# Kernel tuning notes

Hardware: AMD Instinct MI355X
Metric: run time of the kernel (lower is better)

The kernel has to match this reference:

```python
import jax, jax.numpy as jnp
import numpy as np

B, N, C = 4, 4096, 1024
H, M = 16, 64          # num_heads, num_landmarks
DH = C // H
SCALE = H ** (-0.5)    # faithful to source: num_heads**-0.5
LN_EPS = 1e-5


def setup_inputs() -> dict:
    key = jax.random.key(0)
    ks = jax.random.split(key, 8)
    s = 0.02
    return {
        "x": jax.random.normal(ks[0], (B, N, C), jnp.float32),
        "ln_w": jnp.ones((C,), jnp.float32),
        "ln_b": jnp.zeros((C,), jnp.float32),
        "qkv_w": jax.random.normal(ks[1], (3 * C, C), jnp.float32) * s,
        "qkv_b": jax.random.normal(ks[2], (3 * C,), jnp.float32) * s,
        "gamma_w": jax.random.normal(ks[3], (C, C), jnp.float32) * s,
        "gamma_b": jax.random.normal(ks[4], (C,), jnp.float32) * s,
        "proj_w": jax.random.normal(ks[5], (C, C), jnp.float32) * s,
        "proj_b": jax.random.normal(ks[6], (C,), jnp.float32) * s,
    }


def _iterative_inv(K, n_iter=6):
    # Newton-Schulz pseudo-inverse on [..., M, M]
    Id = jnp.eye(K.shape[-1], dtype=K.dtype)
    KA = jnp.abs(K)
    V0 = KA.sum(axis=-2, keepdims=True).max(axis=-1, keepdims=True)
    VI = KA.sum(axis=-1, keepdims=True).max(axis=-2, keepdims=True)
    V = jnp.swapaxes(K, -2, -1) / (V0 * VI)
    for _ in range(n_iter):
        KV = K @ V
        V = 0.25 * V @ (13.0 * Id - KV @ (15.0 * Id - KV @ (7.0 * Id - KV)))
    return V


def reference(x, ln_w, ln_b, qkv_w, qkv_b, gamma_w, gamma_b, proj_w, proj_b):
    # LayerNorm
    mu = x.mean(axis=-1, keepdims=True)
    var = x.var(axis=-1, keepdims=True)
    xn = (x - mu) * jax.lax.rsqrt(var + LN_EPS) * ln_w + ln_b
    # qkv: (B,N,3C) -> (3,B,H,N,DH)
    qkv = (xn @ qkv_w.T + qkv_b).reshape(B, N, 3, H, DH).transpose(2, 0, 3, 1, 4)
    q, k, v = qkv[0], qkv[1], qkv[2]
    # landmarks: mean-pool segments of length N//M, then scale
    q_lm = q.reshape(B, H, M, N // M, DH).mean(axis=-2) * SCALE  # (B,H,M,DH)
    k_lm = k.reshape(B, H, M, N // M, DH).mean(axis=-2) * SCALE
    attn1 = jax.nn.softmax(jnp.einsum('bhnd,bhmd->bhnm', q, k_lm), axis=-1)    # (B,H,N,M)
    attn2 = jax.nn.softmax(jnp.einsum('bhmd,bhld->bhml', q_lm, k_lm), axis=-1)  # (B,H,M,M)
    attn3 = jax.nn.softmax(jnp.einsum('bhmd,bhnd->bhmn', q_lm, k), axis=-1)    # (B,H,M,N)
    attn2_inv = _iterative_inv(attn2)
    out = attn1 @ (attn2_inv @ (attn3 @ v))            # (B,H,N,DH)
    out = out.transpose(0, 2, 1, 3).reshape(B, N, C)
    out = out @ gamma_w.T + gamma_b                    # LipNorm=True branch
    out = out @ proj_w.T + proj_b                      # proj (dropout p=0 is identity)
    return out
```

## Files before the change

### kernel.cpp

```cpp
#include <hip/hip_runtime.h>
#include <stdint.h>

typedef unsigned short u16;
typedef short bf16x8 __attribute__((ext_vector_type(8)));
typedef float f32x4 __attribute__((ext_vector_type(4)));

#define MFMA16(a, b, c) __builtin_amdgcn_mfma_f32_16x16x32_bf16((a), (b), (c), 0, 0, 0)

static __device__ __forceinline__ float bfu2f(u16 u) {
  union { unsigned int i; float f; } z; z.i = ((unsigned int)u) << 16; return z.f;
}
static __device__ __forceinline__ u16 f2bfu(float f) {
  union { float f; unsigned int i; } z; z.f = f;
  unsigned int i = z.i;
  return (u16)((i + 0x7fffu + ((i >> 16) & 1u)) >> 16);
}

__device__ __forceinline__ void gload_lds16(const void* g, void* l) {
  __builtin_amdgcn_global_load_lds((const __attribute__((address_space(1))) void*)g,
                                   (__attribute__((address_space(3))) void*)l, 16, 0, 0);
}

__global__ __launch_bounds__(256) void ln_kernel(
    const float* __restrict__ x, const float* __restrict__ w,
    const float* __restrict__ b, u16* __restrict__ xn) {
  int row = blockIdx.x;
  int t = threadIdx.x;
  const float4* xr = (const float4*)(x + (size_t)row * 1024);
  float4 v = xr[t];
  float s = v.x + v.y + v.z + v.w;
  float ss = v.x * v.x + v.y * v.y + v.z * v.z + v.w * v.w;
#pragma unroll
  for (int m = 1; m < 64; m <<= 1) { s += __shfl_xor(s, m); ss += __shfl_xor(ss, m); }
  __shared__ float sb[4], ssb[4];
  int lane = t & 63, wvi = t >> 6;
  if (lane == 0) { sb[wvi] = s; ssb[wvi] = ss; }
  __syncthreads();
  s = sb[0] + sb[1] + sb[2] + sb[3];
  ss = ssb[0] + ssb[1] + ssb[2] + ssb[3];
  float mu = s * (1.0f / 1024.0f);
  float var = ss * (1.0f / 1024.0f) - mu * mu;
  float rstd = rsqrtf(var + 1e-5f);
  float4 wv4 = ((const float4*)w)[t];
  float4 bv4 = ((const float4*)b)[t];
  ushort4 o;
  o.x = f2bfu((v.x - mu) * rstd * wv4.x + bv4.x);
  o.y = f2bfu((v.y - mu) * rstd * wv4.y + bv4.y);
  o.z = f2bfu((v.z - mu) * rstd * wv4.z + bv4.z);
  o.w = f2bfu((v.w - mu) * rstd * wv4.w + bv4.w);
  ((ushort4*)xn)[(size_t)row * 256 + t] = o;
}

__global__ void cvt3_kernel(const float* __restrict__ a, u16* __restrict__ oa, int na,
                            const float* __restrict__ b, u16* __restrict__ ob, int nb,
                            const float* __restrict__ c, u16* __restrict__ oc, int nc) {
  int total = (na + nb + nc) >> 2;
  for (int i = blockIdx.x * blockDim.x + threadIdx.x; i < total; i += gridDim.x * blockDim.x) {
    int j = i << 2;
    const float* s; u16* d; int off;
    if (j < na) { s = a; d = oa; off = j; }
    else if (j < na + nb) { s = b; d = ob; off = j - na; }
    else { s = c; d = oc; off = j - na - nb; }
    float4 v = *(const float4*)(s + off);
    ushort4 o;
    o.x = f2bfu(v.x); o.y = f2bfu(v.y); o.z = f2bfu(v.z); o.w = f2bfu(v.w);
    *(ushort4*)(d + off) = o;
  }
}

template <int MODE>
__global__ __launch_bounds__(512, 2) void gemm_bt(
    const u16* __restrict__ A, const u16* __restrict__ Bw,
    const float* __restrict__ bias,
    float* __restrict__ Cf, u16* __restrict__ Cb,
    u16* __restrict__ Qo, u16* __restrict__ Ko, u16* __restrict__ Vo,
    int M, int N, int K) {
  __shared__ __attribute__((aligned(16))) u16 As[2][16384];
  __shared__ __attribute__((aligned(16))) u16 Bs[2][16384];
  int tid = threadIdx.x;
  int lane = tid & 63;
  int w = tid >> 6;
  int wr = w >> 2, wc = w & 3;
  int r16 = lane & 15, hi = lane >> 4;
  int l8 = lane >> 3, li = lane & 7;

  int nwg = gridDim.x * gridDim.y;
  int flat = blockIdx.y * gridDim.x + blockIdx.x;
  int q8 = nwg >> 3;
  int swz = (flat & 7) * q8 + (flat >> 3);
  int bx = swz % gridDim.x, by = swz / gridDim.x;

  const char* Abase = (const char*)(A + (size_t)by * 256 * K);
  const char* Bbase = (const char*)(Bw + (size_t)bx * 256 * K);
  size_t rowbytes = (size_t)K * 2;
  int colsw = (li ^ l8) << 4;
  int nkt = K >> 6;

  f32x4 z4 = {0.f, 0.f, 0.f, 0.f};
  f32x4 acc[8][4];
#pragma unroll
  for (int m = 0; m < 8; ++m)
#pragma unroll
    for (int n = 0; n < 4; ++n) acc[m][n] = z4;

#define SG_A(buf, t, r0)                                                      \
  gload_lds16(Abase + (size_t)((r0) + w * 8 + l8) * rowbytes + ((t) << 7) +   \
                  colsw,                                                      \
              (char*)As[buf] + ((r0) + w * 8) * 128)
#define SG_B(buf, t, r0)                                                      \
  gload_lds16(Bbase + (size_t)((r0) + w * 8 + l8) * rowbytes + ((t) << 7) +   \
                  colsw,                                                      \
              (char*)Bs[buf] + ((r0) + w * 8) * 128)

  SG_A(0, 0, 0); SG_A(0, 0, 64); SG_A(0, 0, 128); SG_A(0, 0, 192);
  SG_B(0, 0, 0); SG_B(0, 0, 64); SG_B(0, 0, 128); SG_B(0, 0, 192);
  SG_A(1, 1, 0); SG_A(1, 1, 128); SG_B(1, 1, 0); SG_B(1, 1, 64);
  SG_A(1, 1, 64); SG_A(1, 1, 192);
  asm volatile("s_waitcnt vmcnt(6)" ::: "memory");
  __builtin_amdgcn_s_barrier();
  __builtin_amdgcn_sched_barrier(0);

  int buf = 0;
  bf16x8 af[4][2], bfr[4][2];

#define LDA(mh)                                                               \
  _Pragma("unroll") for (int m = 0; m < 4; ++m) {                             \
    int row = wr * 128 + (mh) * 64 + m * 16 + r16;                            \
    int sw = (row & 7) << 4;                                                  \
    _Pragma("unroll") for (int kk = 0; kk < 2; ++kk)                          \
        af[m][kk] = *(const bf16x8*)(ab + row * 128 +                         \
                                     (((kk << 6) | (hi << 4)) ^ sw));         \
  }
#define LDB(nh)                                                               \
  _Pragma("unroll") for (int n = 0; n < 2; ++n) {                             \
    int row = wc * 64 + (nh) * 32 + n * 16 + r16;                             \
    int sw = (row & 7) << 4;                                                  \
    _Pragma("unroll") for (int kk = 0; kk < 2; ++kk)                          \
        bfr[(nh) * 2 + n][kk] = *(const bf16x8*)(ab2 + row * 128 +            \
                                     (((kk << 6) | (hi << 4)) ^ sw));         \
  }
#define MM(mh, nh)                                                            \
  __builtin_amdgcn_s_setprio(1);                                              \
  _Pragma("unroll") for (int kk = 0; kk < 2; ++kk)                            \
      _Pragma("unroll") for (int m = 0; m < 4; ++m)                           \
          _Pragma("unroll") for (int n = 0; n < 2; ++n)                       \
              acc[(mh) * 4 + m][(nh) * 2 + n] =                               \
      MFMA16(af[m][kk], bfr[(nh) * 2 + n][kk], acc[(mh) * 4 + m][(nh) * 2 + n]); \
  __builtin_amdgcn_s_setprio(0)

#define BAR1                                                                  \
  __builtin_amdgcn_s_barrier();                                               \
  __builtin_amdgcn_sched_barrier(0)
#define BAR2                                                                  \
  __builtin_amdgcn_sched_barrier(0);                                          \
  __builtin_amdgcn_s_barrier();                                               \
  __builtin_amdgcn_sched_barrier(0)

  for (int t = 0; t < nkt; ++t) {
    const char* ab = (const char*)As[buf];
    const char* ab2 = (const char*)Bs[buf];
    bool s1 = (t + 1 < nkt), s2 = (t + 2 < nkt);
    LDA(0);
    LDB(0);
    if (s1) { SG_B(buf ^ 1, t + 1, 128); SG_B(buf ^ 1, t + 1, 192); }
    BAR1;
    MM(0, 0);
    BAR2;
    LDB(1);
    if (s2) { SG_A(buf, t + 2, 0); SG_A(buf, t + 2, 128); }
    BAR1;
    MM(0, 1);
    BAR2;
    LDA(1);
    if (s2) { SG_B(buf, t + 2, 0); SG_B(buf, t + 2, 64); }
    BAR1;
    MM(1, 0);
    BAR2;
    if (s2) { SG_A(buf, t + 2, 64); SG_A(buf, t + 2, 192); }
    BAR1;
    MM(1, 1);
    __builtin_amdgcn_sched_barrier(0);
    if (s2) {
      asm volatile("s_waitcnt vmcnt(6)" ::: "memory");
    } else {
      asm volatile("s_waitcnt vmcnt(0)" ::: "memory");
    }
    __builtin_amdgcn_s_barrier();
    __builtin_amdgcn_sched_barrier(0);
    buf ^= 1;
  }
#undef SG_A
#undef SG_B
#undef LDA
#undef LDB
#undef MM
#undef BAR1
#undef BAR2

#pragma unroll
  for (int m = 0; m < 8; ++m)
#pragma unroll
    for (int n = 0; n < 4; ++n) {
      int row0 = by * 256 + wr * 128 + m * 16 + hi * 4;
      int col = bx * 256 + wc * 64 + n * 16 + r16;
      if (MODE == 2) {
        int jt = col >> 10;
        int h = (col >> 6) & 15, dh = col & 63;
        int bb = row0 >> 12, nt0 = row0 & 4095;
        float bcol = bias[col];
        if (jt == 2) {
          ushort4 o;
          o.x = f2bfu(acc[m][n][0] + bcol);
          o.y = f2bfu(acc[m][n][1] + bcol);
          o.z = f2bfu(acc[m][n][2] + bcol);
          o.w = f2bfu(acc[m][n][3] + bcol);
          *(ushort4*)&Vo[(((size_t)bb * 16 + h) * 64 + dh) * 4096 + nt0] = o;
        } else {
          u16* dst = (jt == 0) ? Qo : Ko;
#pragma unroll
          for (int r = 0; r < 4; ++r)
            dst[(((size_t)bb * 16 + h) * 4096 + nt0 + r) * 64 + dh] =
                f2bfu(acc[m][n][r] + bcol);
        }
      } else {
        float bcol = 0.f;
        if constexpr (MODE != 3) bcol = bias[col];
#pragma unroll
        for (int r = 0; r < 4; ++r) {
          int row = row0 + r;
          float val = acc[m][n][r] + bcol;
          if (MODE == 1) Cf[(size_t)row * N + col] = val;
          else           Cb[(size_t)row * N + col] = f2bfu(val);
        }
      }
    }
}

__global__ __launch_bounds__(64) void landmark_kernel(
    const u16* __restrict__ Q, const u16* __restrict__ K,
    float* __restrict__ qlmf, u16* __restrict__ qlmb,
    float* __restrict__ klmf, u16* __restrict__ klmb) {
  int bm = blockIdx.x;
  int bh = bm >> 6, m = bm & 63;
  int l = threadIdx.x;
  const u16* src = blockIdx.y ? K : Q;
  const u16* base = src + (((size_t)bh * 4096) + m * 64) * 64;
  int r0 = l >> 3;
  int c0 = (l & 7) * 8;
  float s[8] = {};
#pragma unroll
  for (int p = 0; p < 8; ++p) {
    bf16x8 v = *(const bf16x8*)(base + (size_t)(r0 + p * 8) * 64 + c0);
#pragma unroll
    for (int j = 0; j < 8; ++j) s[j] += bfu2f((u16)v[j]);
  }
#pragma unroll
  for (int j = 0; j < 8; ++j) {
    s[j] += __shfl_xor(s[j], 8);
    s[j] += __shfl_xor(s[j], 16);
    s[j] += __shfl_xor(s[j], 32);
  }
  if (l < 8) {
    size_t o = (size_t)bh * 4096 + m * 64 + l * 8;
    float* fo = blockIdx.y ? klmf : qlmf;
    u16* bo = blockIdx.y ? klmb : qlmb;
#pragma unroll
    for (int j = 0; j < 8; ++j) {
      float val = s[j] * (0.25f / 64.0f);
      fo[o + j] = val;
      bo[o + j] = f2bfu(val);
    }
  }
}

__global__ __launch_bounds__(256) void attn3_pv_kernel(
    const u16* __restrict__ qlmb, const u16* __restrict__ Kmat,
    const u16* __restrict__ Vt, float* __restrict__ Upart,
    float* __restrict__ rspart) {
  __shared__ __attribute__((aligned(16))) u16 Elds[4][8192];
  int chunk = blockIdx.x, bh = blockIdx.y;
  int tid = threadIdx.x, lane = tid & 63, w = tid >> 6;
  int r16 = lane & 15, hi = lane >> 4;
  int keybase = chunk * 512 + w * 128;
  const u16* kb = Kmat + ((size_t)bh * 4096 + keybase) * 64;
  const u16* vtb = Vt + (size_t)bh * 262144;
  const u16* qb = qlmb + (size_t)bh * 4096;
  u16* eb = &Elds[w][0];
  f32x4 z4 = {0.f, 0.f, 0.f, 0.f};

  bf16x8 afr[4][2];
#pragma unroll
  for (int m = 0; m < 4; ++m)
#pragma unroll
    for (int kk = 0; kk < 2; ++kk)
      afr[m][kk] = *(const bf16x8*)(qb + (m * 16 + r16) * 64 + kk * 32 + hi * 8);

  float rs[4][4] = {};
  for (int cf = 0; cf < 8; ++cf) {
    f32x4 S[4] = {z4, z4, z4, z4};
#pragma unroll
    for (int kk = 0; kk < 2; ++kk) {
      bf16x8 bfr = *(const bf16x8*)(kb + (size_t)(cf * 16 + r16) * 64 + kk * 32 + hi * 8);
#pragma unroll
      for (int m = 0; m < 4; ++m) S[m] = MFMA16(afr[m][kk], bfr, S[m]);
    }
#pragma unroll
    for (int m = 0; m < 4; ++m)
#pragma unroll
      for (int r = 0; r < 4; ++r) {
        float e = __expf(S[m][r]);
        rs[m][r] += e;
        int row = m * 16 + hi * 4 + r;
        int key = cf * 16 + r16;
        *(u16*)((char*)eb + row * 256 + ((key * 2) ^ ((row & 7) << 4))) = f2bfu(e);
      }
  }
#pragma unroll
  for (int m = 0; m < 4; ++m)
#pragma unroll
    for (int r = 0; r < 4; ++r) {
      float v = rs[m][r];
      v += __shfl_xor(v, 1); v += __shfl_xor(v, 2);
      v += __shfl_xor(v, 4); v += __shfl_xor(v, 8);
      rs[m][r] = v;
    }
  if (r16 == 0) {
    float* rp = rspart + (((size_t)bh * 8 + chunk) * 4 + w) * 64;
#pragma unroll
    for (int m = 0; m < 4; ++m)
#pragma unroll
      for (int r = 0; r < 4; ++r) rp[m * 16 + hi * 4 + r] = rs[m][r];
  }
  __syncthreads();

  f32x4 U[4][4];
#pragma unroll
  for (int m = 0; m < 4; ++m)
#pragma unroll
    for (int df = 0; df < 4; ++df) U[m][df] = z4;
  for (int ks = 0; ks < 4; ++ks) {
    bf16x8 ea[4];
#pragma unroll
    for (int m = 0; m < 4; ++m) {
      int row = m * 16 + r16;
      ea[m] = *(const bf16x8*)((char*)eb + row * 256 + (((ks * 32 + hi * 8) * 2) ^ ((row & 7) << 4)));
    }
#pragma unroll
    for (int df = 0; df < 4; ++df) {
      bf16x8 vb8 = *(const bf16x8*)(vtb + (size_t)(df * 16 + r16) * 4096 +
                                    keybase + ks * 32 + hi * 8);
#pragma unroll
      for (int m = 0; m < 4; ++m) U[m][df] = MFMA16(ea[m], vb8, U[m][df]);
    }
  }
  float* up = Upart + (((size_t)bh * 8 + chunk) * 4 + w) * 4096;
#pragma unroll
  for (int m = 0; m < 4; ++m)
#pragma unroll
    for (int df = 0; df < 4; ++df)
#pragma unroll
      for (int r = 0; r < 4; ++r)
        up[(m * 16 + hi * 4 + r) * 64 + df * 16 + r16] = U[m][df][r];
}

__global__ __launch_bounds__(256) void reduce_t_kernel(
    const float* __restrict__ Upart, const float* __restrict__ rspart,
    float* __restrict__ Tmf) {
  int bh = blockIdx.y;
  int tid = threadIdx.x;
  __shared__ float rsum[64];
  if (tid < 64) {
    float s = 0.f;
    const float* rp = rspart + (size_t)bh * 2048 + tid;
#pragma unroll 8
    for (int p = 0; p < 32; ++p) s += rp[p * 64];
    rsum[tid] = s;
  }
  __syncthreads();
  int idx4 = blockIdx.x * 256 + tid;
  const float4* up = (const float4*)(Upart + (size_t)bh * 131072) + idx4;
  float4 s = {0.f, 0.f, 0.f, 0.f};
#pragma unroll 8
  for (int p = 0; p < 32; ++p) {
    float4 v = up[p * 1024];
    s.x += v.x; s.y += v.y; s.z += v.z; s.w += v.w;
  }
  float inv = 1.0f / rsum[idx4 >> 4];
  s.x *= inv; s.y *= inv; s.z *= inv; s.w *= inv;
  ((float4*)(Tmf + (size_t)bh * 4096))[idx4] = s;
}

__global__ __launch_bounds__(256) void transpose_g_kernel(
    const float* __restrict__ G, u16* __restrict__ GT) {
  __shared__ float t[64][65];
  int tr = blockIdx.y * 64, tc = blockIdx.x * 64;
  int l = threadIdx.x & 63, y = threadIdx.x >> 6;
  for (int r = y; r < 64; r += 4)
    t[r][l] = G[(size_t)(tr + r) * 1024 + tc + l];
  __syncthreads();
  for (int rr = y; rr < 64; rr += 4)
    GT[(size_t)(tc + rr) * 1024 + tr + l] = f2bfu(t[l][rr]);
}

__global__ __launch_bounds__(256) void bias2_kernel(
    const float* __restrict__ P, const float* __restrict__ gb,
    const float* __restrict__ pb, float* __restrict__ b2) {
  int i = blockIdx.x * 256 + threadIdx.x;
  const float4* pr = (const float4*)(P + (size_t)i * 1024);
  const float4* g4 = (const float4*)gb;
  float s = 0.f;
  for (int k = 0; k < 256; ++k) {
    float4 a = pr[k], b = g4[k];
    s += a.x * b.x + a.y * b.y + a.z * b.z + a.w * b.w;
  }
  b2[i] = s + pb[i];
}

__device__ __forceinline__ void mm64(const float (*AT)[68], const float (*Bm)[68],
                                     float (*C)[68], float (*CT)[68],
                                     float alpha, int tid) {
  int tr = (tid >> 4) << 2;
  int tc = (tid & 15) << 2;
  float acc[4][4] = {};
#pragma unroll 4
  for (int k = 0; k < 64; ++k) {
    float4 av = *(const float4*)&AT[k][tr];
    float4 bv = *(const float4*)&Bm[k][tc];
    float aa[4] = {av.x, av.y, av.z, av.w};
    float bb[4] = {bv.x, bv.y, bv.z, bv.w};
#pragma unroll
    for (int i = 0; i < 4; ++i)
#pragma unroll
      for (int j = 0; j < 4; ++j) acc[i][j] = fmaf(aa[i], bb[j], acc[i][j]);
  }
#pragma unroll
  for (int i = 0; i < 4; ++i)
#pragma unroll
    for (int j = 0; j < 4; ++j) {
      float vv = acc[i][j] * alpha;
      C[tr + i][tc + j] = vv;
      if (CT) CT[tc + j][tr + i] = vv;
    }
}

__global__ __launch_bounds__(256) void combine_ns_kernel(
    const float* __restrict__ Tmf, const float* __restrict__ qlmf,
    const float* __restrict__ klmf, u16* __restrict__ WT) {
  __shared__ __attribute__((aligned(16))) float A2T[64][68];
  __shared__ __attribute__((aligned(16))) float Vv[64][68];
  __shared__ __attribute__((aligned(16))) float VT[64][68];
  __shared__ __attribute__((aligned(16))) float KV[64][68];
  __shared__ __attribute__((aligned(16))) float KVT[64][68];
  __shared__ __attribute__((aligned(16))) float T2[64][68];
  __shared__ __attribute__((aligned(16))) float T4[64][68];
  __shared__ __attribute__((aligned(16))) float Tm[64][68];
  __shared__ float redbuf[64];
  __shared__ float v0s, scal;
  int bh = blockIdx.x, tid = threadIdx.x;

  for (int idx = tid; idx < 1024; idx += 256) {
    float4 v = ((const float4*)(Tmf + (size_t)bh * 4096))[idx];
    int r = idx >> 4, c0 = (idx & 15) << 2;
    *(float4*)&Tm[r][c0] = v;
  }
  for (int idx = tid; idx < 4096; idx += 256) {
    int r = idx >> 6, c = idx & 63;
    Vv[c][r] = qlmf[(size_t)bh * 4096 + idx];
    VT[c][r] = klmf[(size_t)bh * 4096 + idx];
  }
  __syncthreads();
  mm64(&Vv[0], &VT[0], &T2[0], nullptr, 1.0f, tid);
  __syncthreads();
  if (tid < 64) {
    float mx = -1e30f;
    for (int c2 = 0; c2 < 64; ++c2) mx = fmaxf(mx, T2[tid][c2]);
    float s = 0.f;
    for (int c2 = 0; c2 < 64; ++c2) { float e = __expf(T2[tid][c2] - mx); T2[tid][c2] = e; s += e; }
    float inv = 1.f / s;
    for (int c2 = 0; c2 < 64; ++c2) { float p = T2[tid][c2] * inv; T2[tid][c2] = p; A2T[c2][tid] = p; }
  }
  __syncthreads();
  if (tid < 64) {
    float cs = 0.f;
    for (int r2 = 0; r2 < 64; ++r2) cs += fabsf(T2[r2][tid]);
    redbuf[tid] = cs;
  }
  __syncthreads();
  if (tid == 0) {
    float v0 = 0.f;
    for (int c2 = 0; c2 < 64; ++c2) v0 = fmaxf(v0, redbuf[c2]);
    v0s = v0;
  }
  __syncthreads();
  if (tid < 64) {
    float rs2 = 0.f;
    for (int c2 = 0; c2 < 64; ++c2) rs2 += fabsf(T2[tid][c2]);
    redbuf[tid] = rs2;
  }
  __syncthreads();
  if (tid == 0) {
    float vi = 0.f;
    for (int r2 = 0; r2 < 64; ++r2) vi = fmaxf(vi, redbuf[r2]);
    scal = 1.0f / (v0s * vi);
  }
  __syncthreads();
  for (int idx = tid; idx < 4096; idx += 256) {
    int r = idx >> 6, c = idx & 63;
    Vv[r][c] = A2T[r][c] * scal;
    VT[r][c] = T2[r][c] * scal;
  }
  __syncthreads();
#pragma unroll 1
  for (int it = 0; it < 6; ++it) {
    mm64(&A2T[0], &Vv[0], &KV[0], &KVT[0], 1.0f, tid);
    __syncthreads();
    for (int idx = tid; idx < 4096; idx += 256) {
      int r = idx >> 6, c = idx & 63;
      T2[r][c] = ((r == c) ? 7.0f : 0.0f) - KV[r][c];
    }
    __syncthreads();
    mm64(&KVT[0], &T2[0], &T4[0], nullptr, 1.0f, tid);
    __syncthreads();
    for (int idx = tid; idx < 4096; idx += 256) {
      int r = idx >> 6, c = idx & 63;
      T2[r][c] = ((r == c) ? 15.0f : 0.0f) - T4[r][c];
    }
    __syncthreads();
    mm64(&KVT[0], &T2[0], &T4[0], nullptr, 1.0f, tid);
    __syncthreads();
    for (int idx = tid; idx < 4096; idx += 256) {
      int r = idx >> 6, c = idx & 63;
      T2[r][c] = ((r == c) ? 13.0f : 0.0f) - T4[r][c];
    }
    __syncthreads();
    mm64(&VT[0], &T2[0], &T4[0], nullptr, 0.25f, tid);
    __syncthreads();
    for (int idx = tid; idx < 4096; idx += 256) {
      int r = idx >> 6, c = idx & 63;
      float vvv = T4[r][c];
      Vv[r][c] = vvv; VT[c][r] = vvv;
    }
    __syncthreads();
  }
  mm64(&VT[0], &Tm[0], &T2[0], nullptr, 1.0f, tid);
  __syncthreads();
  for (int idx = tid; idx < 4096; idx += 256) {
    int r = idx >> 6, c = idx & 63;
    WT[(size_t)bh * 4096 + c * 64 + r] = f2bfu(T2[r][c]);
  }
}

__global__ __launch_bounds__(256) void attn1_out_kernel(
    const u16* __restrict__ Q, const u16* __restrict__ klmb,
    const u16* __restrict__ WT, u16* __restrict__ AO) {
  __shared__ __attribute__((aligned(16))) u16 Elds[4][2048];
  int bh = blockIdx.y;
  int b = bh >> 4, h = bh & 15;
  int tid = threadIdx.x, lane = tid & 63, w = tid >> 6;
  int r16 = lane & 15, hi = lane >> 4;
  int rowbase = blockIdx.x * 128 + w * 32;
  const u16* qb = Q + ((size_t)bh * 4096 + rowbase) * 64;
  const u16* kb = klmb + (size_t)bh * 4096;
  const u16* wtb = WT + (size_t)bh * 4096;
  u16* eb = &Elds[w][0];
  f32x4 z4 = {0.f, 0.f, 0.f, 0.f};

  bf16x8 afr[2][2];
#pragma unroll
  for (int mi = 0; mi < 2; ++mi)
#pragma unroll
    for (int kk = 0; kk < 2; ++kk)
      afr[mi][kk] = *(const bf16x8*)(qb + (mi * 16 + r16) * 64 + kk * 32 + hi * 8);

  float rs[2][4] = {};
  for (int cf = 0; cf < 4; ++cf) {
    f32x4 S[2] = {z4, z4};
#pragma unroll
    for (int kk = 0; kk < 2; ++kk) {
      bf16x8 bfr = *(const bf16x8*)(kb + (cf * 16 + r16) * 64 + kk * 32 + hi * 8);
#pragma unroll
      for (int mi = 0; mi < 2; ++mi) S[mi] = MFMA16(afr[mi][kk], bfr, S[mi]);
    }
#pragma unroll
    for (int mi = 0; mi < 2; ++mi)
#pragma unroll
      for (int r = 0; r < 4; ++r) {
        float e = __expf(S[mi][r]);
        rs[mi][r] += e;
        int row = mi * 16 + hi * 4 + r;
        int key = cf * 16 + r16;
        *(u16*)((char*)eb + row * 128 + ((key * 2) ^ ((row & 7) << 4))) = f2bfu(e);
      }
  }
#pragma unroll
  for (int mi = 0; mi < 2; ++mi)
#pragma unroll
    for (int r = 0; r < 4; ++r) {
      float v = rs[mi][r];
      v += __shfl_xor(v, 1); v += __shfl_xor(v, 2);
      v += __shfl_xor(v, 4); v += __shfl_xor(v, 8);
      rs[mi][r] = v;
    }
  __syncthreads();

  f32x4 O[2][4];
#pragma unroll
  for (int mi = 0; mi < 2; ++mi)
#pragma unroll
    for (int df = 0; df < 4; ++df) O[mi][df] = z4;
  for (int ks = 0; ks < 2; ++ks) {
    bf16x8 ea[2];
#pragma unroll
    for (int mi = 0; mi < 2; ++mi) {
      int row = mi * 16 + r16;
      ea[mi] = *(const bf16x8*)((char*)eb + row * 128 + (((ks * 32 + hi * 8) * 2) ^ ((row & 7) << 4)));
    }
#pragma unroll
    for (int df = 0; df < 4; ++df) {
      bf16x8 wfr = *(const bf16x8*)(wtb + (df * 16 + r16) * 64 + ks * 32 + hi * 8);
#pragma unroll
      for (int mi = 0; mi < 2; ++mi) O[mi][df] = MFMA16(ea[mi], wfr, O[mi][df]);
    }
  }
#pragma unroll
  for (int mi = 0; mi < 2; ++mi)
#pragma unroll
    for (int df = 0; df < 4; ++df)
#pragma unroll
      for (int r = 0; r < 4; ++r) {
        int row = mi * 16 + hi * 4 + r;
        int n = rowbase + row;
        int col = h * 64 + df * 16 + r16;
        float val = O[mi][df][r] / rs[mi][r];
        AO[((size_t)b * 4096 + n) * 1024 + col] = f2bfu(val);
      }
}

extern "C" void kernel_launch(void* const* d_in, const int* in_sizes, int n_in,
                              void* d_out, int out_size, void* d_ws, size_t ws_size,
                              hipStream_t stream) {
  (void)in_sizes; (void)n_in; (void)out_size; (void)ws_size;
  const float* x       = (const float*)d_in[0];
  const float* ln_w    = (const float*)d_in[1];
  const float* ln_b    = (const float*)d_in[2];
  const float* qkv_w   = (const float*)d_in[3];
  const float* qkv_b   = (const float*)d_in[4];
  const float* gamma_w = (const float*)d_in[5];
  const float* gamma_b = (const float*)d_in[6];
  const float* proj_w  = (const float*)d_in[7];
  const float* proj_b  = (const float*)d_in[8];

  char* ws = (char*)d_ws;
  u16* XN     = (u16*)(ws + 0);
  u16* Qb     = (u16*)(ws + 33554432);
  u16* Kb     = (u16*)(ws + 67108864);
  u16* Vb     = (u16*)(ws + 100663296);
  u16* QKVW   = (u16*)(ws + 134217728);
  u16* GW     = (u16*)(ws + 140509184);
  u16* PW     = (u16*)(ws + 142606336);
  float* QLMF = (float*)(ws + 144703488);
  float* KLMF = (float*)(ws + 145752064);
  u16* QLMB   = (u16*)(ws + 146800640);
  u16* KLMB   = (u16*)(ws + 147324928);
  float* RSP  = (float*)(ws + 147849216);
  u16* WTb    = (u16*)(ws + 148373504);
  float* UP   = (float*)XN;
  float* TMF  = (float*)Kb;
  u16* GTb    = (u16*)(ws + 100663296);
  u16* W2b    = (u16*)(ws + 102760448);
  float* B2F  = (float*)(ws + 104857600);

  ln_kernel<<<16384, 256, 0, stream>>>(x, ln_w, ln_b, XN);
  cvt3_kernel<<<2048, 256, 0, stream>>>(qkv_w, QKVW, 3145728,
                                        gamma_w, GW, 1048576,
                                        proj_w, PW, 1048576);
  gemm_bt<2><<<dim3(12, 64), 512, 0, stream>>>(XN, QKVW, qkv_b, nullptr, nullptr,
                                               Qb, Kb, Vb, 16384, 3072, 1024);
  landmark_kernel<<<dim3(4096, 2), 64, 0, stream>>>(Qb, Kb, QLMF, QLMB, KLMF, KLMB);
  attn3_pv_kernel<<<dim3(8, 64), 256, 0, stream>>>(QLMB, Kb, Vb, UP, RSP);
  reduce_t_kernel<<<dim3(4, 64), 256, 0, stream>>>(UP, RSP, TMF);
  transpose_g_kernel<<<dim3(16, 16), 256, 0, stream>>>(gamma_w, GTb);
  gemm_bt<3><<<dim3(4, 4), 512, 0, stream>>>(PW, GTb, nullptr, nullptr, W2b,
                                             nullptr, nullptr, nullptr, 1024, 1024, 1024);
  bias2_kernel<<<4, 256, 0, stream>>>(proj_w, gamma_b, proj_b, B2F);
  combine_ns_kernel<<<64, 256, 0, stream>>>(TMF, QLMF, KLMF, WTb);
  attn1_out_kernel<<<dim3(32, 64), 256, 0, stream>>>(Qb, KLMB, WTb, XN);
  gemm_bt<1><<<dim3(4, 64), 512, 0, stream>>>(XN, W2b, B2F, (float*)d_out, nullptr,
                                              nullptr, nullptr, nullptr, 16384, 1024, 1024);
}
```

Baseline: 403.4 us.

## Split-K the weight-product GEMM and fuse diagonal updates into Newton-Schulz matmuls

The 1024x1024 gamma·proj weight product previously ran as a 16-block GEMM. It now uses a new 8x8x4 split-K kernel with 128x128 tiles, followed by a reduction kernel that sums the four partials into bf16, which should fill far more CUs. In the Newton-Schulz inverse, the 'c*I - X' elementwise passes are folded into the matmul epilogue, and V/VT ping-pong buffers replace the copy pass, removing several syncs and LDS sweeps per iteration. The cost is an extra fp32 partial buffer plus an extra launch and round trip through memory.

```diff
diff --git a/kernel.cpp b/kernel.cpp
--- a/kernel.cpp
+++ b/kernel.cpp
@@ -223,8 +223,7 @@
                 f2bfu(acc[m][n][r] + bcol);
         }
       } else {
-        float bcol = 0.f;
-        if constexpr (MODE != 3) bcol = bias[col];
+        float bcol = bias[col];
 #pragma unroll
         for (int r = 0; r < 4; ++r) {
           int row = row0 + r;
@@ -234,6 +233,85 @@
         }
       }
     }
+}
+
+__global__ __launch_bounds__(256) void w2_kernel(
+    const u16* __restrict__ A, const u16* __restrict__ Bw,
+    float* __restrict__ Cp) {
+  __shared__ __attribute__((aligned(16))) u16 As[8192];
+  __shared__ __attribute__((aligned(16))) u16 Bs[8192];
+  int tid = threadIdx.x, lane = tid & 63, w = tid >> 6;
+  int wr = w >> 1, wc = w & 1;
+  int r16 = lane & 15, hi = lane >> 4;
+  int l8 = lane >> 3, li = lane & 7;
+  int bx = blockIdx.x, by = blockIdx.y, kz = blockIdx.z;
+  const char* Abase = (const char*)(A + (size_t)by * 131072 + kz * 256);
+  const char* Bbase = (const char*)(Bw + (size_t)bx * 131072 + kz * 256);
+  int colsw = (li ^ l8) << 4;
+  f32x4 z4 = {0.f, 0.f, 0.f, 0.f};
+  f32x4 acc[4][4];
+#pragma unroll
+  for (int m = 0; m < 4; ++m)
+#pragma unroll
+    for (int n = 0; n < 4; ++n) acc[m][n] = z4;
+
+  for (int kt = 0; kt < 4; ++kt) {
+    int kb = kt << 7;
+#pragma unroll
+    for (int i = 0; i < 4; ++i) {
+      int c = w * 4 + i;
+      int rr = c * 8 + l8;
+      gload_lds16(Abase + (size_t)rr * 2048 + kb + colsw, (char*)As + c * 1024);
+      gload_lds16(Bbase + (size_t)rr * 2048 + kb + colsw, (char*)Bs + c * 1024);
+    }
+    __syncthreads();
+    int sw = (lane & 7) << 4;
+#pragma unroll
+    for (int kk = 0; kk < 2; ++kk) {
+      int kby = (kk << 6) + (hi << 4);
+      bf16x8 af[4], bfr[4];
+#pragma unroll
+      for (int m = 0; m < 4; ++m) {
+        int row = wr * 64 + m * 16 + r16;
+        af[m] = *(const bf16x8*)((const char*)As + row * 128 + (kby ^ sw));
+      }
+#pragma unroll
+      for (int n = 0; n < 4; ++n) {
+        int row = wc * 64 + n * 16 + r16;
+        bfr[n] = *(const bf16x8*)((const char*)Bs + row * 128 + (kby ^ sw));
+      }
+#pragma unroll
+      for (int m = 0; m < 4; ++m)
+#pragma unroll
+        for (int n = 0; n < 4; ++n) acc[m][n] = MFMA16(af[m], bfr[n], acc[m][n]);
+    }
+    __syncthreads();
+  }
+#pragma unroll
+  for (int m = 0; m < 4; ++m)
+#pragma unroll
+    for (int n = 0; n < 4; ++n)
+#pragma unroll
+      for (int r = 0; r < 4; ++r) {
+        int row = by * 128 + wr * 64 + m * 16 + hi * 4 + r;
+        int col = bx * 128 + wc * 64 + n * 16 + r16;
+        Cp[(size_t)kz * 1048576 + (size_t)row * 1024 + col] = acc[m][n][r];
+      }
+}
+
+__global__ __launch_bounds__(256) void w2_reduce_kernel(
+    const float* __restrict__ Cp, u16* __restrict__ W2b) {
+  int idx4 = blockIdx.x * 256 + threadIdx.x;
+  const float4* p = (const float4*)Cp + idx4;
+  float4 s = p[0];
+  float4 b = p[262144], c = p[524288], d = p[786432];
+  s.x += b.x + c.x + d.x;
+  s.y += b.y + c.y + d.y;
+  s.z += b.z + c.z + d.z;
+  s.w += b.w + c.w + d.w;
+  ushort4 o;
+  o.x = f2bfu(s.x); o.y = f2bfu(s.y); o.z = f2bfu(s.z); o.w = f2bfu(s.w);
+  ((ushort4*)W2b)[idx4] = o;
 }
 
 __global__ __launch_bounds__(64) void landmark_kernel(
@@ -416,9 +494,10 @@
   b2[i] = s + pb[i];
 }
 
-__device__ __forceinline__ void mm64(const float (*AT)[68], const float (*Bm)[68],
-                                     float (*C)[68], float (*CT)[68],
-                                     float alpha, int tid) {
+__device__ __forceinline__ void mm64d(const float (*AT)[68], const float (*Bm)[68],
+                                      float (*C)[68], float (*CT)[68],
+                                      float alpha, float dconst, bool dmode,
+                                      int tid) {
   int tr = (tid >> 4) << 2;
   int tc = (tid & 15) << 2;
   float acc[4][4] = {};
@@ -437,9 +516,10 @@
   for (int i = 0; i < 4; ++i)
 #pragma unroll
     for (int j = 0; j < 4; ++j) {
-      float vv = acc[i][j] * alpha;
-      C[tr + i][tc + j] = vv;
-      if (CT) CT[tc + j][tr + i] = vv;
+      float raw = acc[i][j] * alpha;
+      if (CT) CT[tc + j][tr + i] = raw;
+      C[tr + i][tc + j] =
+          dmode ? (((tr + i) == (tc + j)) ? dconst - raw : -raw) : raw;
     }
 }
 
@@ -469,7 +549,7 @@
     VT[c][r] = klmf[(size_t)bh * 4096 + idx];
   }
   __syncthreads();
-  mm64(&Vv[0], &VT[0], &T2[0], nullptr, 1.0f, tid);
+  mm64d(&Vv[0], &VT[0], &T2[0], nullptr, 1.0f, 0.f, false, tid);
   __syncthreads();
   if (tid < 64) {
     float mx = -1e30f;
@@ -510,39 +590,21 @@
     VT[r][c] = T2[r][c] * scal;
   }
   __syncthreads();
+  float (*Vt_r)[68] = VT;
+  float (*Vt_w)[68] = KV;
 #pragma unroll 1
   for (int it = 0; it < 6; ++it) {
-    mm64(&A2T[0], &Vv[0], &KV[0], &KVT[0], 1.0f, tid);
+    mm64d(&A2T[0], &Vv[0], &T2[0], &KVT[0], 1.0f, 7.0f, true, tid);
     __syncthreads();
-    for (int idx = tid; idx < 4096; idx += 256) {
-      int r = idx >> 6, c = idx & 63;
-      T2[r][c] = ((r == c) ? 7.0f : 0.0f) - KV[r][c];
-    }
+    mm64d(&KVT[0], &T2[0], &T4[0], nullptr, 1.0f, 15.0f, true, tid);
     __syncthreads();
-    mm64(&KVT[0], &T2[0], &T4[0], nullptr, 1.0f, tid);
+    mm64d(&KVT[0], &T4[0], &T2[0], nullptr, 1.0f, 13.0f, true, tid);
     __syncthreads();
-    for (int idx = tid; idx < 4096; idx += 256) {
-      int r = idx >> 6, c = idx & 63;
-      T2[r][c] = ((r == c) ? 15.0f : 0.0f) - T4[r][c];
-    }
+    mm64d(Vt_r, &T2[0], &Vv[0], Vt_w, 0.25f, 0.f, false, tid);
     __syncthreads();
-    mm64(&KVT[0], &T2[0], &T4[0], nullptr, 1.0f, tid);
-    __syncthreads();
-    for (int idx = tid; idx < 4096; idx += 256) {
-      int r = idx >> 6, c = idx & 63;
-      T2[r][c] = ((r == c) ? 13.0f : 0.0f) - T4[r][c];
-    }
-    __syncthreads();
-    mm64(&VT[0], &T2[0], &T4[0], nullptr, 0.25f, tid);
-    __syncthreads();
-    for (int idx = tid; idx < 4096; idx += 256) {
-      int r = idx >> 6, c = idx & 63;
-      float vvv = T4[r][c];
-      Vv[r][c] = vvv; VT[c][r] = vvv;
-    }
-    __syncthreads();
-  }
-  mm64(&VT[0], &Tm[0], &T2[0], nullptr, 1.0f, tid);
+    float (*tmp)[68] = Vt_r; Vt_r = Vt_w; Vt_w = tmp;
+  }
+  mm64d(Vt_r, &Tm[0], &T2[0], nullptr, 1.0f, 0.f, false, tid);
   __syncthreads();
   for (int idx = tid; idx < 4096; idx += 256) {
     int r = idx >> 6, c = idx & 63;
@@ -669,6 +731,7 @@
   u16* GTb    = (u16*)(ws + 100663296);
   u16* W2b    = (u16*)(ws + 102760448);
   float* B2F  = (float*)(ws + 104857600);
+  float* CPF  = (float*)(ws + 109051904);
 
   ln_kernel<<<16384, 256, 0, stream>>>(x, ln_w, ln_b, XN);
   cvt3_kernel<<<2048, 256, 0, stream>>>(qkv_w, QKVW, 3145728,
@@ -680,8 +743,8 @@
   attn3_pv_kernel<<<dim3(8, 64), 256, 0, stream>>>(QLMB, Kb, Vb, UP, RSP);
   reduce_t_kernel<<<dim3(4, 64), 256, 0, stream>>>(UP, RSP, TMF);
   transpose_g_kernel<<<dim3(16, 16), 256, 0, stream>>>(gamma_w, GTb);
-  gemm_bt<3><<<dim3(4, 4), 512, 0, stream>>>(PW, GTb, nullptr, nullptr, W2b,
-                                             nullptr, nullptr, nullptr, 1024, 1024, 1024);
+  w2_kernel<<<dim3(8, 8, 4), 256, 0, stream>>>(PW, GTb, CPF);
+  w2_reduce_kernel<<<1024, 256, 0, stream>>>(CPF, W2b);
   bias2_kernel<<<4, 256, 0, stream>>>(proj_w, gamma_b, proj_b, B2F);
   combine_ns_kernel<<<64, 256, 0, stream>>>(TMF, QLMF, KLMF, WTb);
   attn1_out_kernel<<<dim3(32, 64), 256, 0, stream>>>(Qb, KLMB, WTb, XN);
```

Result: faster. 377.4 us (-6.4%).
